# Performance work log

Hardware: AMD Instinct MI355X
Metric: run time of the kernel (lower is better)

## Reference

```python
import jax, jax.numpy as jnp
import numpy as np

BN_EPS = 1e-5

def _bn(y, g, b, m, v):
    # inference-mode BatchNorm2d over channel axis 1
    scale = g / jnp.sqrt(v + BN_EPS)
    return (y - m[None, :, None, None]) * scale[None, :, None, None] + b[None, :, None, None]

def setup_inputs() -> dict:
    key = jax.random.key(0)
    ks = jax.random.split(key, 16)
    b, c, h, w = 4, 64, 256, 512
    kc = 32
    return {
        "x": jax.random.normal(ks[0], (b, c, h, w), dtype=jnp.float32),
        "Wq": jax.random.normal(ks[1], (kc, c), dtype=jnp.float32) * 0.05,
        "bnq_g": jax.random.uniform(ks[2], (kc,), dtype=jnp.float32),
        "bnq_b": jax.random.normal(ks[3], (kc,), dtype=jnp.float32) * 0.1,
        "bnq_m": jax.random.normal(ks[4], (kc,), dtype=jnp.float32) * 0.1,
        "bnq_v": jax.random.uniform(ks[5], (kc,), dtype=jnp.float32) + 0.5,
        "Wk": jax.random.normal(ks[6], (kc, c), dtype=jnp.float32) * 0.05,
        "bnk_g": jax.random.uniform(ks[7], (kc,), dtype=jnp.float32),
        "bnk_b": jax.random.normal(ks[8], (kc,), dtype=jnp.float32) * 0.1,
        "bnk_m": jax.random.normal(ks[9], (kc,), dtype=jnp.float32) * 0.1,
        "bnk_v": jax.random.uniform(ks[10], (kc,), dtype=jnp.float32) + 0.5,
        "Wv": jax.random.normal(ks[11], (c, c), dtype=jnp.float32) * 0.05,
        "bv": jax.random.normal(ks[12], (c,), dtype=jnp.float32) * 0.1,
        "gamma": jax.random.normal(ks[13], (1,), dtype=jnp.float32) * 0.1,
    }

def reference(x, Wq, bnq_g, bnq_b, bnq_m, bnq_v, Wk, bnk_g, bnk_b, bnk_m, bnk_v, Wv, bv, gamma):
    # x: [b,c,h,w]. Vertical (height-axis) attention, independent per (batch, column).
    q = _bn(jnp.einsum('kc,bchw->bkhw', Wq, x), bnq_g, bnq_b, bnq_m, bnq_v)  # [b,kc,h,w]
    k = _bn(jnp.einsum('kc,bchw->bkhw', Wk, x), bnk_g, bnk_b, bnk_m, bnk_v)  # [b,kc,h,w]
    # score1 = Q[b,w,h,kc] @ K[b,w,kc,h] -> [b,w,h,h]
    score = jnp.einsum('bkhw,bkgw->bwhg', q, k)
    attn = jax.nn.softmax(score, axis=-1)  # softmax over key height g
    v = jnp.einsum('dc,bchw->bdhw', Wv, x) + bv[None, :, None, None]  # [b,c,h,w]
    buf = jnp.einsum('bwhg,bdgw->bdhw', attn, v)  # [b,c,h,w]
    return gamma * buf + x  # out_add branch
```

## Files before the change

kernel.cpp:

```cpp
#include <hip/hip_runtime.h>
#include <hip/hip_bf16.h>

#define BB 4
#define CC 64
#define HH 256
#define WW 512
#define KCC 32
#define PLANE (HH*WW)

typedef __attribute__((ext_vector_type(8))) __bf16 bf16x8;
typedef __attribute__((ext_vector_type(4))) __bf16 bf16x4;
typedef __attribute__((ext_vector_type(2))) __bf16 bf16x2;
typedef __attribute__((ext_vector_type(4))) float floatx4;

__device__ __forceinline__ float bf2f(unsigned short u) {
    union { unsigned v; float f; } x; x.v = ((unsigned)u) << 16; return x.f;
}

__device__ __forceinline__ void async_copy16(const float* gp, float* lp) {
    __builtin_amdgcn_global_load_lds(
        (const __attribute__((address_space(1))) unsigned int*)gp,
        (__attribute__((address_space(3))) unsigned int*)lp,
        16, 0, 0);
}

__global__ __launch_bounds__(256, 2)
void proj_kernel(const float* __restrict__ x,
                 const float* __restrict__ Wq, const float* __restrict__ Wk,
                 const float* __restrict__ Wv, const float* __restrict__ bv,
                 const float* __restrict__ bnq_g, const float* __restrict__ bnq_b,
                 const float* __restrict__ bnq_m, const float* __restrict__ bnq_v,
                 const float* __restrict__ bnk_g, const float* __restrict__ bnk_b,
                 const float* __restrict__ bnk_m, const float* __restrict__ bnk_v,
                 unsigned short* __restrict__ Qb, unsigned short* __restrict__ Kb,
                 unsigned short* __restrict__ Vb)
{
    __shared__ __align__(16) float sStageF[8192];
    __shared__ __align__(16) unsigned short sX[8 * 256 * 8];

    unsigned short* sYQ = (unsigned short*)sStageF;
    unsigned short* sYK = sYQ + 16 * 40;
    unsigned short* sYVb = sYK + 16 * 40;

    const int tid  = threadIdx.x;
    const int lane = tid & 63, wv = tid >> 6;
    const int quad = lane >> 4, lr = lane & 15;
    const int bid  = blockIdx.x;
    const int b = bid >> 9, rem = bid & 511;
    const int h0 = (rem >> 5) << 4;
    const int w0 = (rem & 31) << 4;

    const float* xtile = x + (size_t)b * CC * PLANE + (size_t)h0 * WW + w0;
    const int s_lh = lane >> 2, s_ww = lane & 3;
    const int p_lw = tid & 15, p_lh = tid >> 4;
    const int chs = ((p_lw << 4) | (p_lh ^ p_lw)) * 8;

#pragma unroll
    for (int it = 0; it < 8; ++it) {
        const int cl = it * 4 + wv;
        async_copy16(xtile + (size_t)cl * PLANE + s_lh * WW + s_ww * 4,
                     &sStageF[cl * 256 + lane * 4]);
    }

    const int nmt = (wv >= 2) ? 4 : 2;
    const float* Wsrc = (wv == 0) ? Wq : (wv == 1) ? Wk : Wv;
    bf16x8 wf[4][2];
#pragma unroll
    for (int mt = 0; mt < 4; ++mt) {
        if (mt >= nmt) break;
#pragma unroll
        for (int ks = 0; ks < 2; ++ks) {
            const float* p = Wsrc + (mt * 16 + lr) * CC + ks * 32 + quad * 8;
            bf16x8 v;
#pragma unroll
            for (int j = 0; j < 8; ++j) v[j] = (__bf16)p[j];
            wf[mt][ks] = v;
        }
    }
    float s8[2][4], b8[4][4];
    if (wv == 0) {
#pragma unroll
        for (int mt = 0; mt < 2; ++mt)
#pragma unroll
            for (int i = 0; i < 4; ++i) {
                int chn = mt * 16 + quad * 4 + i;
                float s = bnq_g[chn] * rsqrtf(bnq_v[chn] + 1e-5f);
                s8[mt][i] = s; b8[mt][i] = bnq_b[chn] - bnq_m[chn] * s;
            }
    } else if (wv == 1) {
#pragma unroll
        for (int mt = 0; mt < 2; ++mt)
#pragma unroll
            for (int i = 0; i < 4; ++i) {
                int chn = mt * 16 + quad * 4 + i;
                float s = bnk_g[chn] * rsqrtf(bnk_v[chn] + 1e-5f);
                s8[mt][i] = s; b8[mt][i] = bnk_b[chn] - bnk_m[chn] * s;
            }
    } else {
#pragma unroll
        for (int mt = 0; mt < 4; ++mt)
#pragma unroll
            for (int i = 0; i < 4; ++i)
                b8[mt][i] = bv[mt * 16 + quad * 4 + i];
    }

    __syncthreads();
#pragma unroll
    for (int cc = 0; cc < 4; ++cc) {
        bf16x8 v;
#pragma unroll
        for (int j = 0; j < 8; ++j)
            v[j] = (__bf16)sStageF[(cc * 8 + j) * 256 + p_lh * 16 + p_lw];
        *(bf16x8*)&sX[cc * 2048 + chs] = v;
    }
    __syncthreads();

#pragma unroll
    for (int it = 0; it < 8; ++it) {
        const int cl = it * 4 + wv;
        async_copy16(xtile + (size_t)(32 + cl) * PLANE + s_lh * WW + s_ww * 4,
                     &sStageF[cl * 256 + lane * 4]);
    }
    __syncthreads();
#pragma unroll
    for (int cc = 0; cc < 4; ++cc) {
        bf16x8 v;
#pragma unroll
        for (int j = 0; j < 8; ++j)
            v[j] = (__bf16)sStageF[(cc * 8 + j) * 256 + p_lh * 16 + p_lw];
        *(bf16x8*)&sX[(4 + cc) * 2048 + chs] = v;
    }
    __syncthreads();

    const floatx4 zed = {0.f, 0.f, 0.f, 0.f};

    if (wv < 2) {
        unsigned short* sYw = (wv == 0) ? sYQ : sYK;
        unsigned short* Db  = (wv == 0) ? Qb  : Kb;
        const int p2 = lane >> 2, seg = lane & 3;
        for (int nt = 0; nt < 16; ++nt) {
            const int ch = (nt * 16 + (lr ^ nt)) * 8;
            bf16x8 xb0 = *(const bf16x8*)&sX[quad * 2048 + ch];
            bf16x8 xb1 = *(const bf16x8*)&sX[(4 + quad) * 2048 + ch];
#pragma unroll
            for (int mt = 0; mt < 2; ++mt) {
                floatx4 acc = zed;
                acc = __builtin_amdgcn_mfma_f32_16x16x32_bf16(wf[mt][0], xb0, acc, 0, 0, 0);
                acc = __builtin_amdgcn_mfma_f32_16x16x32_bf16(wf[mt][1], xb1, acc, 0, 0, 0);
                bf16x4 y;
#pragma unroll
                for (int i = 0; i < 4; ++i) y[i] = (__bf16)(acc[i] * s8[mt][i] + b8[mt][i]);
                *(bf16x4*)&sYw[lr * 40 + mt * 16 + quad * 4] = y;
            }
            uint4 v = *(const uint4*)&sYw[p2 * 40 + seg * 8];
            *(uint4*)&Db[((size_t)(b * WW + w0 + nt) * HH + h0 + p2) * KCC + seg * 8] = v;
        }
    } else {
        unsigned short* sYw = sYVb + (wv - 2) * (16 * 72);
        const int base_nt = (wv - 2) * 8;
        for (int n8 = 0; n8 < 8; ++n8) {
            const int nt = base_nt + n8;
            const int ch = (nt * 16 + (lr ^ nt)) * 8;
            bf16x8 xb0 = *(const bf16x8*)&sX[quad * 2048 + ch];
            bf16x8 xb1 = *(const bf16x8*)&sX[(4 + quad) * 2048 + ch];
#pragma unroll
            for (int mt = 0; mt < 4; ++mt) {
                floatx4 acc = zed;
                acc = __builtin_amdgcn_mfma_f32_16x16x32_bf16(wf[mt][0], xb0, acc, 0, 0, 0);
                acc = __builtin_amdgcn_mfma_f32_16x16x32_bf16(wf[mt][1], xb1, acc, 0, 0, 0);
                bf16x4 y;
#pragma unroll
                for (int i = 0; i < 4; ++i) y[i] = (__bf16)(acc[i] + b8[mt][i]);
                *(bf16x4*)&sYw[lr * 72 + mt * 16 + quad * 4] = y;
            }
            const size_t vbase = ((size_t)(b * WW + w0 + nt) * HH + h0) * CC;
#pragma unroll
            for (int r = 0; r < 2; ++r) {
                int idx = r * 64 + lane;
                int pos = idx >> 3, sg = idx & 7;
                uint4 v = *(const uint4*)&sYw[pos * 72 + sg * 8];
                *(uint4*)&Vb[vbase + pos * CC + sg * 8] = v;
            }
        }
    }
}

__global__ __launch_bounds__(512, 4)
void attn_kernel(const unsigned short* __restrict__ Qb,
                 const unsigned short* __restrict__ Kb,
                 const unsigned short* __restrict__ Vb,
                 const float* __restrict__ gamma,
                 unsigned short* __restrict__ Ob)
{
    __shared__ __align__(16) unsigned short sVf[16384];
    __shared__ __align__(16) unsigned short sP[8][1280];
    __shared__ float sL[256];

    const int tid = threadIdx.x, lane = tid & 63, wv = tid >> 6;
    const int quad = lane >> 4, lr = lane & 15;
    const int col = blockIdx.x;

    const unsigned short* Qg = Qb + (size_t)col * HH * KCC;
    const unsigned short* Kg = Kb + (size_t)col * HH * KCC;
    const unsigned short* Vg = Vb + (size_t)col * HH * CC;

    bf16x8 qf[2], kf[16];
#pragma unroll
    for (int ht = 0; ht < 2; ++ht)
        qf[ht] = *(const bf16x8*)&Qg[(wv * 32 + ht * 16 + lr) * KCC + quad * 8];
#pragma unroll
    for (int gt = 0; gt < 16; ++gt)
        kf[gt] = *(const bf16x8*)&Kg[(gt * 16 + lr) * KCC + quad * 8];

    unsigned short* sVp = &sP[0][0];
    for (int half = 0; half < 2; ++half) {
#pragma unroll
        for (int it = 0; it < 2; ++it) {
            int idx = it * 512 + tid;
            int gr = idx >> 3, sg = idx & 7;
            *(uint4*)&sVp[gr * CC + sg * 8] =
                *(const uint4*)&Vg[(size_t)(half * 128 + gr) * CC + sg * 8];
        }
        __syncthreads();
#pragma unroll
        for (int it = 0; it < 2; ++it) {
            int id = it * 512 + tid;
            int go = id >> 6, d = id & 63;
            bf16x8 v;
#pragma unroll
            for (int j = 0; j < 8; ++j)
                ((unsigned short*)&v)[j] = sVp[(go * 8 + j) * CC + d];
            *(bf16x8*)&sVf[((half * 16 + go) * 64 + d) * 8] = v;
        }
        __syncthreads();
    }

    floatx4 O[2][4];
#pragma unroll
    for (int a = 0; a < 2; ++a)
#pragma unroll
        for (int dd = 0; dd < 4; ++dd) O[a][dd] = (floatx4){0.f, 0.f, 0.f, 0.f};
    float lpart[2] = {0.f, 0.f};

    unsigned short* sPw = sP[wv];
    const floatx4 zed = {0.f, 0.f, 0.f, 0.f};

#pragma unroll
    for (int ch = 0; ch < 8; ++ch) {
#pragma unroll
        for (int gt = 0; gt < 2; ++gt) {
#pragma unroll
            for (int ht = 0; ht < 2; ++ht) {
                floatx4 s = __builtin_amdgcn_mfma_f32_16x16x32_bf16(kf[ch * 2 + gt], qf[ht], zed, 0, 0, 0);
                float p0 = __expf(s[0]), p1 = __expf(s[1]), p2 = __expf(s[2]), p3 = __expf(s[3]);
                lpart[ht] += (p0 + p1) + (p2 + p3);
                bf16x2 pa = {(__bf16)p0, (__bf16)p1};
                bf16x2 pb = {(__bf16)p2, (__bf16)p3};
                int base = (ht * 16 + lr) * 40 + gt * 16 + quad * 4;
                *(bf16x2*)&sPw[base]     = pa;
                *(bf16x2*)&sPw[base + 2] = pb;
            }
        }
        bf16x8 paf[2];
#pragma unroll
        for (int ht = 0; ht < 2; ++ht)
            paf[ht] = *(const bf16x8*)&sPw[(ht * 16 + lr) * 40 + quad * 8];
#pragma unroll
        for (int dt = 0; dt < 4; ++dt) {
            bf16x8 vf = *(const bf16x8*)&sVf[((ch * 4 + quad) * 64 + dt * 16 + lr) * 8];
#pragma unroll
            for (int ht = 0; ht < 2; ++ht)
                O[ht][dt] = __builtin_amdgcn_mfma_f32_16x16x32_bf16(paf[ht], vf, O[ht][dt], 0, 0, 0);
        }
    }

    const float gm = gamma[0];
#pragma unroll
    for (int ht = 0; ht < 2; ++ht) {
        float l = lpart[ht];
        l += __shfl_xor(l, 16, 64);
        l += __shfl_xor(l, 32, 64);
        if (lane < 16) sL[wv * 32 + ht * 16 + lane] = gm / l;
    }

#pragma unroll
    for (int ht = 0; ht < 2; ++ht) {
        float f0 = sL[wv * 32 + ht * 16 + quad * 4 + 0];
        float f1 = sL[wv * 32 + ht * 16 + quad * 4 + 1];
        float f2 = sL[wv * 32 + ht * 16 + quad * 4 + 2];
        float f3 = sL[wv * 32 + ht * 16 + quad * 4 + 3];
#pragma unroll
        for (int dt = 0; dt < 4; ++dt) {
            floatx4 o = O[ht][dt];
            int cb = dt * 16 + lr;
            *(__bf16*)&sPw[(quad * 4 + 0) * 72 + cb] = (__bf16)(o[0] * f0);
            *(__bf16*)&sPw[(quad * 4 + 1) * 72 + cb] = (__bf16)(o[1] * f1);
            *(__bf16*)&sPw[(quad * 4 + 2) * 72 + cb] = (__bf16)(o[2] * f2);
            *(__bf16*)&sPw[(quad * 4 + 3) * 72 + cb] = (__bf16)(o[3] * f3);
        }
#pragma unroll
        for (int it = 0; it < 2; ++it) {
            int idx = it * 64 + lane;
            int hr = idx >> 3, sg = idx & 7;
            uint4 v = *(const uint4*)&sPw[hr * 72 + sg * 8];
            *(uint4*)&Ob[(size_t)(col * HH + wv * 32 + ht * 16 + hr) * CC + sg * 8] = v;
        }
    }
}

__global__ __launch_bounds__(256)
void add_kernel(const unsigned short* __restrict__ Ob,
                const float* __restrict__ x,
                float* __restrict__ out)
{
    __shared__ __align__(16) unsigned short sT[64 * 72];
    const int tid = threadIdx.x;
    const int bid = blockIdx.x;
    const int b = bid >> 11, rem = bid & 2047, h = rem >> 3, w0 = (rem & 7) << 6;

#pragma unroll
    for (int it = 0; it < 2; ++it) {
        int idx = it * 256 + tid;
        int tw = idx >> 3, sg = idx & 7;
        uint4 v = *(const uint4*)&Ob[(size_t)((b * WW + w0 + tw) * HH + h) * CC + sg * 8];
        *(uint4*)&sT[tw * 72 + sg * 8] = v;
    }
    __syncthreads();

    const int d = tid >> 2, ws = tid & 3;
    const size_t base = ((size_t)(b * CC + d)) * PLANE + h * WW + w0 + ws * 16;
    const float* xp = x + base;
    float* op = out + base;
#pragma unroll
    for (int k = 0; k < 4; ++k) {
        float4 xv = *(const float4*)&xp[k * 4];
        float4 r;
        r.x = bf2f(sT[(ws * 16 + k * 4 + 0) * 72 + d]) + xv.x;
        r.y = bf2f(sT[(ws * 16 + k * 4 + 1) * 72 + d]) + xv.y;
        r.z = bf2f(sT[(ws * 16 + k * 4 + 2) * 72 + d]) + xv.z;
        r.w = bf2f(sT[(ws * 16 + k * 4 + 3) * 72 + d]) + xv.w;
        *(float4*)&op[k * 4] = r;
    }
}

#define KSTR 40
#define VSTR 72
__device__ __forceinline__ float bflo(unsigned u) { union { unsigned v; float f; } x; x.v = u << 16; return x.f; }
__device__ __forceinline__ float bfhi(unsigned u) { union { unsigned v; float f; } x; x.v = u & 0xffff0000u; return x.f; }

__global__ __launch_bounds__(256, 1)
void vattn_fused(const float* __restrict__ x,
                 const float* __restrict__ Wq,
                 const float* __restrict__ bnq_g, const float* __restrict__ bnq_b,
                 const float* __restrict__ bnq_m, const float* __restrict__ bnq_v,
                 const float* __restrict__ Wk,
                 const float* __restrict__ bnk_g, const float* __restrict__ bnk_b,
                 const float* __restrict__ bnk_m, const float* __restrict__ bnk_v,
                 const float* __restrict__ Wv, const float* __restrict__ bv,
                 const float* __restrict__ gamma,
                 float* __restrict__ out)
{
    __shared__ __align__(16) __hip_bfloat16 sK[HH * KSTR];
    __shared__ __align__(16) __hip_bfloat16 sV2[HH * VSTR];
    const int t = threadIdx.x;
    const int bw = blockIdx.x;
    const int b = bw / WW, w = bw % WW;
    const size_t plane = (size_t)HH * WW;
    const float* xp = x + (size_t)b * CC * plane + (size_t)t * WW + w;
    float xr[CC];
#pragma unroll
    for (int c = 0; c < CC; ++c) xr[c] = xp[(size_t)c * plane];
    float qr[KCC];
#pragma unroll
    for (int j = 0; j < KCC; ++j) {
        float aq = 0.f, ak = 0.f;
#pragma unroll
        for (int c = 0; c < CC; ++c) { aq += Wq[j * CC + c] * xr[c]; ak += Wk[j * CC + c] * xr[c]; }
        const float sq = bnq_g[j] * rsqrtf(bnq_v[j] + 1e-5f);
        const float sk = bnk_g[j] * rsqrtf(bnk_v[j] + 1e-5f);
        qr[j] = (aq - bnq_m[j]) * sq + bnq_b[j];
        sK[t * KSTR + j] = __float2bfloat16((ak - bnk_m[j]) * sk + bnk_b[j]);
    }
#pragma unroll
    for (int d = 0; d < CC; ++d) {
        float av = bv[d];
#pragma unroll
        for (int c = 0; c < CC; ++c) av += Wv[d * CC + c] * xr[c];
        sV2[t * VSTR + d] = __float2bfloat16(av);
    }
    __syncthreads();
    float o[CC];
#pragma unroll
    for (int d = 0; d < CC; ++d) o[d] = 0.f;
    float l = 0.f;
    for (int g = 0; g < HH; ++g) {
        const uint4* kp = (const uint4*)(sK + g * KSTR);
        float s = 0.f;
#pragma unroll
        for (int i = 0; i < 4; ++i) {
            const uint4 kk = kp[i];
            s += bflo(kk.x) * qr[i * 8 + 0] + bfhi(kk.x) * qr[i * 8 + 1]
               + bflo(kk.y) * qr[i * 8 + 2] + bfhi(kk.y) * qr[i * 8 + 3]
               + bflo(kk.z) * qr[i * 8 + 4] + bfhi(kk.z) * qr[i * 8 + 5]
               + bflo(kk.w) * qr[i * 8 + 6] + bfhi(kk.w) * qr[i * 8 + 7];
        }
        const float p = __expf(s);
        l += p;
        const uint4* vp = (const uint4*)(sV2 + g * VSTR);
#pragma unroll
        for (int i = 0; i < 8; ++i) {
            const uint4 vv = vp[i];
            o[i * 8 + 0] += p * bflo(vv.x); o[i * 8 + 1] += p * bfhi(vv.x);
            o[i * 8 + 2] += p * bflo(vv.y); o[i * 8 + 3] += p * bfhi(vv.y);
            o[i * 8 + 4] += p * bflo(vv.z); o[i * 8 + 5] += p * bfhi(vv.z);
            o[i * 8 + 6] += p * bflo(vv.w); o[i * 8 + 7] += p * bfhi(vv.w);
        }
    }
    const float gm = gamma[0];
    const float rl = 1.f / l;
    float* op = out + (size_t)b * CC * plane + (size_t)t * WW + w;
#pragma unroll
    for (int d = 0; d < CC; ++d) op[(size_t)d * plane] = gm * (o[d] * rl) + xr[d];
}

extern "C" void kernel_launch(void* const* d_in, const int* in_sizes, int n_in,
                              void* d_out, int out_size, void* d_ws, size_t ws_size,
                              hipStream_t stream) {
    const float* x     = (const float*)d_in[0];
    const float* Wq    = (const float*)d_in[1];
    const float* bnq_g = (const float*)d_in[2];
    const float* bnq_b = (const float*)d_in[3];
    const float* bnq_m = (const float*)d_in[4];
    const float* bnq_v = (const float*)d_in[5];
    const float* Wk    = (const float*)d_in[6];
    const float* bnk_g = (const float*)d_in[7];
    const float* bnk_b = (const float*)d_in[8];
    const float* bnk_m = (const float*)d_in[9];
    const float* bnk_v = (const float*)d_in[10];
    const float* Wv    = (const float*)d_in[11];
    const float* bv    = (const float*)d_in[12];
    const float* gamma = (const float*)d_in[13];
    float* out = (float*)d_out;

    const size_t need = 201326592;
    if (ws_size >= need) {
        unsigned short* Qb = (unsigned short*)d_ws;
        unsigned short* Kb = Qb + 16777216;
        unsigned short* Vb = Kb + 16777216;
        unsigned short* Ob = Vb + 33554432;
        hipLaunchKernelGGL(proj_kernel, dim3(2048), dim3(256), 0, stream,
                           x, Wq, Wk, Wv, bv,
                           bnq_g, bnq_b, bnq_m, bnq_v,
                           bnk_g, bnk_b, bnk_m, bnk_v,
                           Qb, Kb, Vb);
        hipLaunchKernelGGL(attn_kernel, dim3(2048), dim3(512), 0, stream,
                           Qb, Kb, Vb, gamma, Ob);
        hipLaunchKernelGGL(add_kernel, dim3(8192), dim3(256), 0, stream,
                           Ob, x, out);
    } else {
        hipLaunchKernelGGL(vattn_fused, dim3(BB * WW), dim3(HH), 0, stream,
                           x, Wq, bnq_g, bnq_b, bnq_m, bnq_v,
                           Wk, bnk_g, bnk_b, bnk_m, bnk_v,
                           Wv, bv, gamma, out);
    }
}
```

Baseline: 423.6 us.

## Make projection kernel persistent over four tiles with prefetched x loads

The projection kernel now runs 512 blocks of 512 threads, each handling four consecutive 16x16 spatial tiles. It stages all 64 input channels at once and issues the async load of the next tile's x while the MFMA projections for the current tile run. Work is spread over eight waves, two each for Q and K and four for V. This is meant to hide global-load latency behind compute, at the cost of more LDS per block, lower occupancy (one 512-thread block per launch bound) and fewer blocks in the grid.

```diff
diff --git a/kernel.cpp b/kernel.cpp
--- a/kernel.cpp
+++ b/kernel.cpp
@@ -24,7 +24,7 @@
         16, 0, 0);
 }
 
-__global__ __launch_bounds__(256, 2)
+__global__ __launch_bounds__(512, 1)
 void proj_kernel(const float* __restrict__ x,
                  const float* __restrict__ Wq, const float* __restrict__ Wk,
                  const float* __restrict__ Wv, const float* __restrict__ bv,
@@ -35,35 +35,34 @@
                  unsigned short* __restrict__ Qb, unsigned short* __restrict__ Kb,
                  unsigned short* __restrict__ Vb)
 {
-    __shared__ __align__(16) float sStageF[8192];
+    __shared__ __align__(16) float sStageF[64 * 256];
     __shared__ __align__(16) unsigned short sX[8 * 256 * 8];
-
-    unsigned short* sYQ = (unsigned short*)sStageF;
-    unsigned short* sYK = sYQ + 16 * 40;
-    unsigned short* sYVb = sYK + 16 * 40;
+    __shared__ __align__(16) unsigned short sY[8][16 * 72];
 
     const int tid  = threadIdx.x;
     const int lane = tid & 63, wv = tid >> 6;
     const int quad = lane >> 4, lr = lane & 15;
-    const int bid  = blockIdx.x;
-    const int b = bid >> 9, rem = bid & 511;
-    const int h0 = (rem >> 5) << 4;
-    const int w0 = (rem & 31) << 4;
-
-    const float* xtile = x + (size_t)b * CC * PLANE + (size_t)h0 * WW + w0;
     const int s_lh = lane >> 2, s_ww = lane & 3;
-    const int p_lw = tid & 15, p_lh = tid >> 4;
-    const int chs = ((p_lw << 4) | (p_lh ^ p_lw)) * 8;
-
-#pragma unroll
-    for (int it = 0; it < 8; ++it) {
-        const int cl = it * 4 + wv;
-        async_copy16(xtile + (size_t)cl * PLANE + s_lh * WW + s_ww * 4,
-                     &sStageF[cl * 256 + lane * 4]);
-    }
-
-    const int nmt = (wv >= 2) ? 4 : 2;
-    const float* Wsrc = (wv == 0) ? Wq : (wv == 1) ? Wk : Wv;
+    const int pos  = tid & 255, phalf = tid >> 8;
+    const int p_lw = pos & 15, p_lh = pos >> 4;
+    const int chs  = ((p_lw << 4) | (p_lh ^ p_lw)) * 8;
+
+    const int nmt = (wv >= 4) ? 4 : 2;
+    const float* Wsrc = (wv < 2) ? Wq : (wv < 4) ? Wk : Wv;
+
+    {
+        const int gt0 = blockIdx.x * 4;
+        const int b = gt0 >> 9, rem = gt0 & 511;
+        const float* xg = x + (size_t)b * CC * PLANE
+                        + (size_t)((rem >> 5) << 4) * WW + ((rem & 31) << 4);
+#pragma unroll
+        for (int it = 0; it < 8; ++it) {
+            const int cl = it * 8 + wv;
+            async_copy16(xg + (size_t)cl * PLANE + s_lh * WW + s_ww * 4,
+                         &sStageF[cl * 256 + lane * 4]);
+        }
+    }
+
     bf16x8 wf[4][2];
 #pragma unroll
     for (int mt = 0; mt < 4; ++mt) {
@@ -78,7 +77,7 @@
         }
     }
     float s8[2][4], b8[4][4];
-    if (wv == 0) {
+    if (wv < 2) {
 #pragma unroll
         for (int mt = 0; mt < 2; ++mt)
 #pragma unroll
@@ -87,7 +86,7 @@
                 float s = bnq_g[chn] * rsqrtf(bnq_v[chn] + 1e-5f);
                 s8[mt][i] = s; b8[mt][i] = bnq_b[chn] - bnq_m[chn] * s;
             }
-    } else if (wv == 1) {
+    } else if (wv < 4) {
 #pragma unroll
         for (int mt = 0; mt < 2; ++mt)
 #pragma unroll
@@ -104,82 +103,89 @@
                 b8[mt][i] = bv[mt * 16 + quad * 4 + i];
     }
 
-    __syncthreads();
-#pragma unroll
-    for (int cc = 0; cc < 4; ++cc) {
-        bf16x8 v;
-#pragma unroll
-        for (int j = 0; j < 8; ++j)
-            v[j] = (__bf16)sStageF[(cc * 8 + j) * 256 + p_lh * 16 + p_lw];
-        *(bf16x8*)&sX[cc * 2048 + chs] = v;
-    }
-    __syncthreads();
-
-#pragma unroll
-    for (int it = 0; it < 8; ++it) {
-        const int cl = it * 4 + wv;
-        async_copy16(xtile + (size_t)(32 + cl) * PLANE + s_lh * WW + s_ww * 4,
-                     &sStageF[cl * 256 + lane * 4]);
-    }
-    __syncthreads();
-#pragma unroll
-    for (int cc = 0; cc < 4; ++cc) {
-        bf16x8 v;
-#pragma unroll
-        for (int j = 0; j < 8; ++j)
-            v[j] = (__bf16)sStageF[(cc * 8 + j) * 256 + p_lh * 16 + p_lw];
-        *(bf16x8*)&sX[(4 + cc) * 2048 + chs] = v;
-    }
-    __syncthreads();
-
     const floatx4 zed = {0.f, 0.f, 0.f, 0.f};
-
-    if (wv < 2) {
-        unsigned short* sYw = (wv == 0) ? sYQ : sYK;
-        unsigned short* Db  = (wv == 0) ? Qb  : Kb;
-        const int p2 = lane >> 2, seg = lane & 3;
-        for (int nt = 0; nt < 16; ++nt) {
-            const int ch = (nt * 16 + (lr ^ nt)) * 8;
-            bf16x8 xb0 = *(const bf16x8*)&sX[quad * 2048 + ch];
-            bf16x8 xb1 = *(const bf16x8*)&sX[(4 + quad) * 2048 + ch];
-#pragma unroll
-            for (int mt = 0; mt < 2; ++mt) {
-                floatx4 acc = zed;
-                acc = __builtin_amdgcn_mfma_f32_16x16x32_bf16(wf[mt][0], xb0, acc, 0, 0, 0);
-                acc = __builtin_amdgcn_mfma_f32_16x16x32_bf16(wf[mt][1], xb1, acc, 0, 0, 0);
-                bf16x4 y;
-#pragma unroll
-                for (int i = 0; i < 4; ++i) y[i] = (__bf16)(acc[i] * s8[mt][i] + b8[mt][i]);
-                *(bf16x4*)&sYw[lr * 40 + mt * 16 + quad * 4] = y;
-            }
-            uint4 v = *(const uint4*)&sYw[p2 * 40 + seg * 8];
-            *(uint4*)&Db[((size_t)(b * WW + w0 + nt) * HH + h0 + p2) * KCC + seg * 8] = v;
-        }
-    } else {
-        unsigned short* sYw = sYVb + (wv - 2) * (16 * 72);
-        const int base_nt = (wv - 2) * 8;
-        for (int n8 = 0; n8 < 8; ++n8) {
-            const int nt = base_nt + n8;
-            const int ch = (nt * 16 + (lr ^ nt)) * 8;
-            bf16x8 xb0 = *(const bf16x8*)&sX[quad * 2048 + ch];
-            bf16x8 xb1 = *(const bf16x8*)&sX[(4 + quad) * 2048 + ch];
-#pragma unroll
-            for (int mt = 0; mt < 4; ++mt) {
-                floatx4 acc = zed;
-                acc = __builtin_amdgcn_mfma_f32_16x16x32_bf16(wf[mt][0], xb0, acc, 0, 0, 0);
-                acc = __builtin_amdgcn_mfma_f32_16x16x32_bf16(wf[mt][1], xb1, acc, 0, 0, 0);
-                bf16x4 y;
-#pragma unroll
-                for (int i = 0; i < 4; ++i) y[i] = (__bf16)(acc[i] + b8[mt][i]);
-                *(bf16x4*)&sYw[lr * 72 + mt * 16 + quad * 4] = y;
-            }
-            const size_t vbase = ((size_t)(b * WW + w0 + nt) * HH + h0) * CC;
-#pragma unroll
-            for (int r = 0; r < 2; ++r) {
-                int idx = r * 64 + lane;
-                int pos = idx >> 3, sg = idx & 7;
-                uint4 v = *(const uint4*)&sYw[pos * 72 + sg * 8];
-                *(uint4*)&Vb[vbase + pos * CC + sg * 8] = v;
+    unsigned short* sYw = sY[wv];
+    const int p2 = lane >> 2, seg = lane & 3;
+
+    for (int t = 0; t < 4; ++t) {
+        const int gt = blockIdx.x * 4 + t;
+        const int b = gt >> 9, rem = gt & 511;
+        const int h0 = (rem >> 5) << 4, w0 = (rem & 31) << 4;
+
+        __syncthreads();
+
+#pragma unroll
+        for (int cc = 0; cc < 4; ++cc) {
+            const int g = phalf * 4 + cc;
+            bf16x8 v;
+#pragma unroll
+            for (int j = 0; j < 8; ++j)
+                v[j] = (__bf16)sStageF[(g * 8 + j) * 256 + p_lh * 16 + p_lw];
+            *(bf16x8*)&sX[g * 2048 + chs] = v;
+        }
+        __syncthreads();
+
+        if (t < 3) {
+            const int gt1 = gt + 1;
+            const int b1 = gt1 >> 9, rem1 = gt1 & 511;
+            const float* xg = x + (size_t)b1 * CC * PLANE
+                            + (size_t)((rem1 >> 5) << 4) * WW + ((rem1 & 31) << 4);
+#pragma unroll
+            for (int it = 0; it < 8; ++it) {
+                const int cl = it * 8 + wv;
+                async_copy16(xg + (size_t)cl * PLANE + s_lh * WW + s_ww * 4,
+                             &sStageF[cl * 256 + lane * 4]);
+            }
+        }
+
+        if (wv < 4) {
+            unsigned short* Db = (wv < 2) ? Qb : Kb;
+            const int ntb = (wv & 1) << 3;
+#pragma unroll
+            for (int i = 0; i < 8; ++i) {
+                const int nt = ntb + i;
+                const int ch = (nt * 16 + (lr ^ nt)) * 8;
+                bf16x8 xb0 = *(const bf16x8*)&sX[quad * 2048 + ch];
+                bf16x8 xb1 = *(const bf16x8*)&sX[(4 + quad) * 2048 + ch];
+#pragma unroll
+                for (int mt = 0; mt < 2; ++mt) {
+                    floatx4 acc = zed;
+                    acc = __builtin_amdgcn_mfma_f32_16x16x32_bf16(wf[mt][0], xb0, acc, 0, 0, 0);
+                    acc = __builtin_amdgcn_mfma_f32_16x16x32_bf16(wf[mt][1], xb1, acc, 0, 0, 0);
+                    bf16x4 y;
+#pragma unroll
+                    for (int k = 0; k < 4; ++k) y[k] = (__bf16)(acc[k] * s8[mt][k] + b8[mt][k]);
+                    *(bf16x4*)&sYw[lr * 72 + mt * 16 + quad * 4] = y;
+                }
+                uint4 v = *(const uint4*)&sYw[p2 * 72 + seg * 8];
+                *(uint4*)&Db[((size_t)(b * WW + w0 + nt) * HH + h0 + p2) * KCC + seg * 8] = v;
+            }
+        } else {
+            const int ntb = (wv - 4) << 2;
+#pragma unroll
+            for (int i = 0; i < 4; ++i) {
+                const int nt = ntb + i;
+                const int ch = (nt * 16 + (lr ^ nt)) * 8;
+                bf16x8 xb0 = *(const bf16x8*)&sX[quad * 2048 + ch];
+                bf16x8 xb1 = *(const bf16x8*)&sX[(4 + quad) * 2048 + ch];
+#pragma unroll
+                for (int mt = 0; mt < 4; ++mt) {
+                    floatx4 acc = zed;
+                    acc = __builtin_amdgcn_mfma_f32_16x16x32_bf16(wf[mt][0], xb0, acc, 0, 0, 0);
+                    acc = __builtin_amdgcn_mfma_f32_16x16x32_bf16(wf[mt][1], xb1, acc, 0, 0, 0);
+                    bf16x4 y;
+#pragma unroll
+                    for (int k = 0; k < 4; ++k) y[k] = (__bf16)(acc[k] + b8[mt][k]);
+                    *(bf16x4*)&sYw[lr * 72 + mt * 16 + quad * 4] = y;
+                }
+                const size_t vbase = ((size_t)(b * WW + w0 + nt) * HH + h0) * CC;
+#pragma unroll
+                for (int r = 0; r < 2; ++r) {
+                    int idx = r * 64 + lane;
+                    int ps = idx >> 3, sg = idx & 7;
+                    uint4 v = *(const uint4*)&sYw[ps * 72 + sg * 8];
+                    *(uint4*)&Vb[vbase + ps * CC + sg * 8] = v;
+                }
             }
         }
     }
@@ -448,7 +454,7 @@
         unsigned short* Kb = Qb + 16777216;
         unsigned short* Vb = Kb + 16777216;
         unsigned short* Ob = Vb + 33554432;
-        hipLaunchKernelGGL(proj_kernel, dim3(2048), dim3(256), 0, stream,
+        hipLaunchKernelGGL(proj_kernel, dim3(512), dim3(512), 0, stream,
                            x, Wq, Wk, Wv, bv,
                            bnq_g, bnq_b, bnq_m, bnq_v,
                            bnk_g, bnk_b, bnk_m, bnk_v,
```

After: 414.0 us. 2.3% less time.
